# Optimization experiments

Measured on AMD Instinct MI355X. Metric: run time of the kernel, lower is better.

## Reference

```python
import jax, jax.numpy as jnp
import numpy as np

NEG_INF = -1e9  # matches torch masked_fill value of -1000000000.0


def setup_inputs() -> dict:
    key = jax.random.key(0)
    k1, k2, k3, k4 = jax.random.split(key, 4)
    B, H, S, D = 4, 16, 2048, 128
    query = jax.random.normal(k1, (B, H, S, D), dtype=jnp.float32)
    key_t = jax.random.normal(k2, (B, H, S, D), dtype=jnp.float32)
    value = jax.random.normal(k3, (B, H, S, D), dtype=jnp.float32)
    mask = jax.random.randint(k4, (B, 1, 1, S), 0, 2, dtype=jnp.int32)
    return {"query": query, "key": key_t, "value": value, "mask": mask, "dropout": 0}


def reference(query, key, value, mask, dropout):
    # scores = Q K^T / sqrt(d_k)   [B,H,S,S]
    d_k = query.shape[-1]
    scores = jnp.einsum("bhqd,bhkd->bhqk", query, key) / jnp.sqrt(jnp.asarray(d_k, query.dtype))
    # masked_fill_(mask == 0, -1e9); mask broadcasts [B,1,1,S] -> [B,H,S,S]
    scores = jnp.where(mask == 0, jnp.asarray(NEG_INF, scores.dtype), scores)
    # dropout == 0 -> identity (deterministic reference / eval mode)
    attn = jax.nn.softmax(scores, axis=-1)
    return jnp.einsum("bhqk,bhkd->bhqd", attn, value)
```

## Files before the change

kernel.cpp:

```cpp
#include <hip/hip_runtime.h>
#include <hip/hip_bf16.h>

#define S_LEN 2048
#define D_DIM 128
#define QBLK 128
#define KVBLK 32
#define NT (S_LEN / KVBLK)
#define KCHUNK 8192
#define VCHUNK 8192
#define PRE_BYTES ((size_t)64 * NT * (KCHUNK + VCHUNK))

typedef __attribute__((ext_vector_type(8))) short short8v;
typedef __attribute__((ext_vector_type(16))) float f32x16;

static __device__ __forceinline__ unsigned f2bf2(float lo, float hi) {
    float2 f2; f2.x = lo; f2.y = hi;
    __hip_bfloat162 h2 = __float22bfloat162_rn(f2);
    unsigned r;
    __builtin_memcpy(&r, &h2, 4);
    return r;
}

static __device__ __forceinline__ void plswap(unsigned& a, unsigned& b) {
    auto r = __builtin_amdgcn_permlane32_swap(a, b, false, false);
    a = r[0]; b = r[1];
}
static __device__ __forceinline__ float plswap_sum(float x) {
    unsigned a = __float_as_uint(x), b = a;
    plswap(a, b);
    return __uint_as_float(a) + __uint_as_float(b);
}

static __device__ __forceinline__ void gload16(const void* g, void* l) {
    __builtin_amdgcn_global_load_lds(
        (const __attribute__((address_space(1))) unsigned int*)g,
        (__attribute__((address_space(3))) unsigned int*)l,
        16, 0, 0);
}

static __device__ __forceinline__ void stage8k(const unsigned char* g, unsigned char* l,
                                               int wv, int lane) {
#pragma unroll
    for (int i = 0; i < 2; ++i) {
        const int off = (wv * 2 + i) * 1024;
        gload16(g + off + lane * 16, l + off);
    }
}

#define VTS 133

__global__ __launch_bounds__(256) void preconv(
    const float* __restrict__ Kp, const float* __restrict__ Vp,
    unsigned short* __restrict__ Ko, unsigned short* __restrict__ Vo)
{
    __shared__ float vt[64 * VTS];
    const int tid = threadIdx.x;
    const int blk = blockIdx.x;
    const size_t gbase = (size_t)(blk >> 5) * S_LEN * D_DIM + (size_t)(blk & 31) * 64 * D_DIM;

#pragma unroll
    for (int i = 0; i < 8; ++i) {
        int idx = (tid + 256 * i) * 4;
        int row = idx >> 7, col = idx & 127;
        float4 v4 = *(const float4*)(Vp + gbase + idx);
        float* d = &vt[row * VTS + col];
        d[0] = v4.x; d[1] = v4.y; d[2] = v4.z; d[3] = v4.w;
    }

    unsigned short* kout = Ko + (size_t)blk * 8192;
#pragma unroll
    for (int i = 0; i < 4; ++i) {
        int o = tid + 256 * i;
        int row = o >> 4, bs = o & 15;
        int b = (bs & 8) | ((bs ^ row) & 7);
        const float* gp = Kp + gbase + row * D_DIM + 8 * b;
        float4 x = *(const float4*)gp;
        float4 y = *(const float4*)(gp + 4);
        uint4 w;
        w.x = f2bf2(x.x, x.y); w.y = f2bf2(x.z, x.w);
        w.z = f2bf2(y.x, y.y); w.w = f2bf2(y.z, y.w);
        *(uint4*)(kout + o * 8) = w;
    }
    __syncthreads();

    unsigned short* vout = Vo + (size_t)blk * 8192;
#pragma unroll
    for (int i = 0; i < 4; ++i) {
        int u = tid + 256 * i;
        int ch = u >> 9, r = u & 511;
        int d = r >> 2, bs = r & 3;
        int b = bs ^ ((d >> 1) & 3);
        const float* c0 = &vt[(ch * 32 + 8 * b) * VTS + d];
        uint4 w;
        w.x = f2bf2(c0[0 * VTS], c0[1 * VTS]);
        w.y = f2bf2(c0[2 * VTS], c0[3 * VTS]);
        w.z = f2bf2(c0[4 * VTS], c0[5 * VTS]);
        w.w = f2bf2(c0[6 * VTS], c0[7 * VTS]);
        *(uint4*)(vout + u * 8) = w;
    }
}

#define ASMEM (3 * KCHUNK + 3 * VCHUNK + 8192)

__global__ __launch_bounds__(256, 2) void sdpa_fwd_pre(
    const float* __restrict__ Qp, const unsigned short* __restrict__ Kpre,
    const unsigned short* __restrict__ Vpre, const int* __restrict__ Mp,
    float* __restrict__ Op)
{
    extern __shared__ unsigned char smem[];
    unsigned char* KbB = smem;
    unsigned char* VbB = smem + 3 * KCHUNK;
    float* blds = (float*)(smem + 3 * KCHUNK + 3 * VCHUNK);

    const int tid  = threadIdx.x;
    const int lane = tid & 63;
    const int wv   = tid >> 6;
    const int h    = lane >> 5;
    const int c31  = lane & 31;
    const int hrx  = h ^ (c31 & 7);
    const int vsx  = (c31 >> 1) & 3;
    const int lbid = ((blockIdx.x & 7) << 7) | (blockIdx.x >> 3);
    const int bh   = lbid >> 4;
    const int q0   = (lbid & 15) * QBLK;
    const int bb   = bh >> 4;
    const size_t base = (size_t)bh * S_LEN * D_DIM;
    const unsigned char* Kg = (const unsigned char*)Kpre + (size_t)bh * (NT * KCHUNK);
    const unsigned char* Vg = (const unsigned char*)Vpre + (size_t)bh * (NT * VCHUNK);

    constexpr float SC   = 0.08838834764831845f * 1.4426950408889634f;
    constexpr float NEGB = -1.4426950408889634e9f;
    constexpr float M2   = 16.0f;

    {
        const int* mp = Mp + bb * S_LEN;
#pragma unroll
        for (int i = 0; i < S_LEN / 256; ++i)
            blds[tid + 256 * i] = mp[tid + 256 * i] ? -M2 : NEGB;
    }

    short8v qf[8];
    {
        const float* qrp = Qp + base + (size_t)(q0 + 32 * wv + c31) * D_DIM;
#pragma unroll
        for (int kk = 0; kk < 8; ++kk) {
            float4 x = *(const float4*)(qrp + 16 * kk + 8 * h);
            float4 y = *(const float4*)(qrp + 16 * kk + 8 * h + 4);
            uint4 w;
            w.x = f2bf2(x.x * SC, x.y * SC); w.y = f2bf2(x.z * SC, x.w * SC);
            w.z = f2bf2(y.x * SC, y.y * SC); w.w = f2bf2(y.z * SC, y.w * SC);
            *(uint4*)&qf[kk] = w;
        }
    }

    stage8k(Kg, KbB, wv, lane);
    stage8k(Vg, VbB, wv, lane);
    stage8k(Kg + KCHUNK, KbB + KCHUNK, wv, lane);
    stage8k(Vg + VCHUNK, VbB + VCHUNK, wv, lane);
    asm volatile("s_waitcnt vmcnt(4) lgkmcnt(0)" ::: "memory");
    __builtin_amdgcn_s_barrier();

    f32x16 acc[4];
#pragma unroll
    for (int dt = 0; dt < 4; ++dt)
#pragma unroll
        for (int i = 0; i < 16; ++i) acc[dt][i] = 0.f;

    float lpart = 0.f;
    int cur = 0;

#pragma unroll 1
    for (int t0 = 0; t0 < NT; ++t0) {
        const unsigned char* KcB = KbB + cur * KCHUNK;
        const unsigned char* VcB = VbB + cur * VCHUNK;

        const bool pf = (t0 + 2 < NT);
        if (pf) {
            int stg = cur + 2; if (stg >= 3) stg -= 3;
            stage8k(Kg + (size_t)(t0 + 2) * KCHUNK, KbB + stg * KCHUNK, wv, lane);
            stage8k(Vg + (size_t)(t0 + 2) * VCHUNK, VbB + stg * VCHUNK, wv, lane);
        }

        f32x16 s;
        {
            const float* bp = blds + t0 * KVBLK + 4 * h;
#pragma unroll
            for (int t4 = 0; t4 < 4; ++t4) {
                float4 b4 = *(const float4*)(bp + 8 * t4);
                s[4 * t4 + 0] = b4.x; s[4 * t4 + 1] = b4.y;
                s[4 * t4 + 2] = b4.z; s[4 * t4 + 3] = b4.w;
            }
        }

        {
            const unsigned char* rowp = KcB + (c31 << 8);
#pragma unroll
            for (int kk = 0; kk < 8; ++kk) {
                const int bs = ((2 * kk) & 8) | (((2 * kk) & 7) ^ hrx);
                short8v kf = *(const short8v*)(rowp + (bs << 4));
                s = __builtin_amdgcn_mfma_f32_32x32x16_bf16(kf, qf[kk], s, 0, 0, 0);
            }
        }

        unsigned w0[4], w1[4];
#pragma unroll
        for (int t4 = 0; t4 < 4; ++t4) {
            float e0 = __builtin_amdgcn_exp2f(s[4 * t4 + 0]);
            float e1 = __builtin_amdgcn_exp2f(s[4 * t4 + 1]);
            float e2 = __builtin_amdgcn_exp2f(s[4 * t4 + 2]);
            float e3 = __builtin_amdgcn_exp2f(s[4 * t4 + 3]);
            w0[t4] = f2bf2(e0, e1);
            w1[t4] = f2bf2(e2, e3);
            lpart += (e0 + e1) + (e2 + e3);
        }

#pragma unroll
        for (int kk = 0; kk < 2; ++kk) {
            unsigned ax = w0[2 * kk], bx = w0[2 * kk + 1];
            plswap(ax, bx);
            unsigned ay = w1[2 * kk], by = w1[2 * kk + 1];
            plswap(ay, by);
            uint4 pw;
            pw.x = ax; pw.y = ay; pw.z = bx; pw.w = by;
            short8v pfv = *(short8v*)&pw;
            const int bs = (2 * kk + h) ^ vsx;
#pragma unroll
            for (int dt = 0; dt < 4; ++dt) {
                short8v vf = *(const short8v*)(VcB + ((32 * dt + c31) << 6) + (bs << 4));
                acc[dt] = __builtin_amdgcn_mfma_f32_32x32x16_bf16(vf, pfv, acc[dt], 0, 0, 0);
            }
        }

        if (pf) {
            asm volatile("s_waitcnt vmcnt(4)" ::: "memory");
        } else {
            asm volatile("s_waitcnt vmcnt(0)" ::: "memory");
        }
        __builtin_amdgcn_s_barrier();
        cur = (cur + 1 == 3) ? 0 : cur + 1;
    }

    const float linv = 1.0f / plswap_sum(lpart);
    float* sw = (float*)(smem + wv * (32 * 68 * 4));
#pragma unroll
    for (int ph = 0; ph < 2; ++ph) {
#pragma unroll
        for (int dp = 0; dp < 2; ++dp) {
            const int dtg = 2 * ph + dp;
#pragma unroll
            for (int r = 0; r < 16; ++r) {
                int dloc = 32 * dp + (r & 3) + 8 * (r >> 2) + 4 * h;
                sw[c31 * 68 + dloc] = acc[dtg][r] * linv;
            }
        }
#pragma unroll
        for (int it = 0; it < 8; ++it) {
            int f4 = lane + 64 * it;
            int qq = f4 >> 4, c4 = f4 & 15;
            float4 val = *(const float4*)&sw[qq * 68 + 4 * c4];
            *(float4*)(Op + base + (size_t)(q0 + 32 * wv + qq) * D_DIM + 64 * ph + 4 * c4) = val;
        }
    }
}

#define FBKV 64
#define FBNT (S_LEN / FBKV)
#define FBQB 128
#define KSTRIDE 136
#define VSTRIDE 72
#define KELEMS (FBKV * KSTRIDE)
#define VELEMS (D_DIM * VSTRIDE)
#define KBYTES (2 * KELEMS * 2)
#define VBYTES (2 * VELEMS * 2)
#define FBSMEM (KBYTES + VBYTES + S_LEN * 4)

struct KReg { float4 a[4][2]; };
struct VReg { float4 a[2][4]; };

static __device__ __forceinline__ void load_K(KReg& kr, const float* Kbase,
                                              int kv0, int kr0, int kc8) {
#pragma unroll
    for (int i = 0; i < 4; ++i) {
        const float* gp = Kbase + (size_t)(kv0 + kr0 + 16 * i) * D_DIM + 8 * kc8;
        kr.a[i][0] = *(const float4*)gp;
        kr.a[i][1] = *(const float4*)(gp + 4);
    }
}
static __device__ __forceinline__ void write_K(const KReg& kr, unsigned short* Kn,
                                               int kr0, int kc8) {
#pragma unroll
    for (int i = 0; i < 4; ++i) {
        uint4 w;
        w.x = f2bf2(kr.a[i][0].x, kr.a[i][0].y);
        w.y = f2bf2(kr.a[i][0].z, kr.a[i][0].w);
        w.z = f2bf2(kr.a[i][1].x, kr.a[i][1].y);
        w.w = f2bf2(kr.a[i][1].z, kr.a[i][1].w);
        *(uint4*)&Kn[(kr0 + 16 * i) * KSTRIDE + 8 * kc8] = w;
    }
}
static __device__ __forceinline__ void load_V(VReg& vr, const float* Vbase,
                                              int kv0, int vkq, int vdg) {
#pragma unroll
    for (int ii = 0; ii < 2; ++ii)
#pragma unroll
        for (int r = 0; r < 4; ++r)
            vr.a[ii][r] = *(const float4*)(Vbase + (size_t)(kv0 + 4 * vkq + 32 * ii + r) * D_DIM + 4 * vdg);
}
static __device__ __forceinline__ void write_V(const VReg& vr, unsigned short* Vn,
                                               int vkq, int vdg) {
#pragma unroll
    for (int ii = 0; ii < 2; ++ii) {
        const int kvb = 4 * vkq + 32 * ii;
        const int d0  = 4 * vdg;
        uint2 u;
        u.x = f2bf2(vr.a[ii][0].x, vr.a[ii][1].x); u.y = f2bf2(vr.a[ii][2].x, vr.a[ii][3].x);
        *(uint2*)&Vn[(d0 + 0) * VSTRIDE + kvb] = u;
        u.x = f2bf2(vr.a[ii][0].y, vr.a[ii][1].y); u.y = f2bf2(vr.a[ii][2].y, vr.a[ii][3].y);
        *(uint2*)&Vn[(d0 + 1) * VSTRIDE + kvb] = u;
        u.x = f2bf2(vr.a[ii][0].z, vr.a[ii][1].z); u.y = f2bf2(vr.a[ii][2].z, vr.a[ii][3].z);
        *(uint2*)&Vn[(d0 + 2) * VSTRIDE + kvb] = u;
        u.x = f2bf2(vr.a[ii][0].w, vr.a[ii][1].w); u.y = f2bf2(vr.a[ii][2].w, vr.a[ii][3].w);
        *(uint2*)&Vn[(d0 + 3) * VSTRIDE + kvb] = u;
    }
}

__global__ __launch_bounds__(256, 2) void sdpa_fwd_fb(
    const float* __restrict__ Qp, const float* __restrict__ Kp,
    const float* __restrict__ Vp, const int* __restrict__ Mp,
    float* __restrict__ Op)
{
    extern __shared__ unsigned char smem[];
    unsigned short* Kb   = (unsigned short*)smem;
    unsigned short* Vb   = (unsigned short*)(smem + KBYTES);
    float*          mlds = (float*)(smem + KBYTES + VBYTES);

    const int tid  = threadIdx.x;
    const int lane = tid & 63;
    const int wv   = tid >> 6;
    const int h    = lane >> 5;
    const int c31  = lane & 31;
    const int bid  = blockIdx.x;
    const int bh   = bid >> 4;
    const int q0   = (bid & 15) * FBQB;
    const int bb   = bh >> 4;
    const size_t base = (size_t)bh * S_LEN * D_DIM;

    constexpr float SC   = 0.08838834764831845f * 1.4426950408889634f;
    constexpr float NEGB = -1.4426950408889634e9f;
    constexpr float THR  = 11.541560327111708f;

    {
        const int* mp = Mp + bb * S_LEN;
#pragma unroll
        for (int i = 0; i < S_LEN / 256; ++i)
            mlds[tid + 256 * i] = mp[tid + 256 * i] ? 0.f : NEGB;
    }

    short8v qf[8];
    {
        const float* qrp = Qp + base + (size_t)(q0 + 32 * wv + c31) * D_DIM;
#pragma unroll
        for (int kk = 0; kk < 8; ++kk) {
            float4 x = *(const float4*)(qrp + 16 * kk + 8 * h);
            float4 y = *(const float4*)(qrp + 16 * kk + 8 * h + 4);
            uint4 w;
            w.x = f2bf2(x.x, x.y); w.y = f2bf2(x.z, x.w);
            w.z = f2bf2(y.x, y.y); w.w = f2bf2(y.z, y.w);
            *(uint4*)&qf[kk] = w;
        }
    }

    const int kc8 = tid & 15;
    const int kr0 = tid >> 4;
    const int vdg = tid & 31;
    const int vkq = tid >> 5;

    {
        KReg kr; VReg vr;
        load_K(kr, Kp + base, 0, kr0, kc8);
        load_V(vr, Vp + base, 0, vkq, vdg);
        write_K(kr, Kb, kr0, kc8);
        write_V(vr, Vb, vkq, vdg);
    }
    __syncthreads();

    f32x16 acc[4];
#pragma unroll
    for (int dt = 0; dt < 4; ++dt)
#pragma unroll
        for (int i = 0; i < 16; ++i) acc[dt][i] = 0.f;

    float m2 = -INFINITY;
    float lsum = 0.f;
    int cur = 0;

#pragma unroll 1
    for (int t0 = 0; t0 < FBNT; ++t0) {
        const int kv0 = t0 * FBKV;
        unsigned short* Kc = Kb + cur * KELEMS;
        unsigned short* Vc = Vb + cur * VELEMS;
        unsigned short* Kn = Kb + (cur ^ 1) * KELEMS;
        unsigned short* Vn = Vb + (cur ^ 1) * VELEMS;
        const bool pf = (t0 + 1 < FBNT);

        KReg kr; VReg vr;
        if (pf) {
            load_K(kr, Kp + base, kv0 + FBKV, kr0, kc8);
            load_V(vr, Vp + base, kv0 + FBKV, vkq, vdg);
        }

        f32x16 stc[2];
#pragma unroll
        for (int c = 0; c < 2; ++c) {
            f32x16 s;
#pragma unroll
            for (int i = 0; i < 16; ++i) s[i] = 0.f;
#pragma unroll
            for (int kk = 0; kk < 8; ++kk) {
                short8v kf = *(const short8v*)&Kc[(32 * c + c31) * KSTRIDE + 16 * kk + 8 * h];
                s = __builtin_amdgcn_mfma_f32_32x32x16_bf16(kf, qf[kk], s, 0, 0, 0);
            }
            stc[c] = s;
        }

        float p[2][16];
#pragma unroll
        for (int c = 0; c < 2; ++c)
#pragma unroll
            for (int t = 0; t < 4; ++t) {
                float4 b4 = *(const float4*)&mlds[kv0 + 32 * c + 8 * t + 4 * h];
                p[c][4 * t + 0] = fmaf(stc[c][4 * t + 0], SC, b4.x);
                p[c][4 * t + 1] = fmaf(stc[c][4 * t + 1], SC, b4.y);
                p[c][4 * t + 2] = fmaf(stc[c][4 * t + 2], SC, b4.z);
                p[c][4 * t + 3] = fmaf(stc[c][4 * t + 3], SC, b4.w);
            }

        float pmax = -INFINITY;
#pragma unroll
        for (int c = 0; c < 2; ++c)
#pragma unroll
            for (int r = 0; r < 16; ++r) pmax = fmaxf(pmax, p[c][r]);
        pmax = fmaxf(pmax, __shfl_xor(pmax, 32));
        if (!__all(pmax <= m2 + THR)) {
            float mnew = fmaxf(m2, pmax);
            float fr = __builtin_amdgcn_exp2f(m2 - mnew);
            m2 = mnew;
            lsum *= fr;
#pragma unroll
            for (int dt = 0; dt < 4; ++dt)
#pragma unroll
                for (int i = 0; i < 16; ++i) acc[dt][i] *= fr;
        }
        float ssum = 0.f;
#pragma unroll
        for (int c = 0; c < 2; ++c)
#pragma unroll
            for (int r = 0; r < 16; ++r) {
                float e = __builtin_amdgcn_exp2f(p[c][r] - m2);
                p[c][r] = e; ssum += e;
            }
        ssum += __shfl_xor(ssum, 32);
        lsum += ssum;

        unsigned w0[2][4], w1[2][4];
#pragma unroll
        for (int c = 0; c < 2; ++c)
#pragma unroll
            for (int t = 0; t < 4; ++t) {
                w0[c][t] = f2bf2(p[c][4 * t + 0], p[c][4 * t + 1]);
                w1[c][t] = f2bf2(p[c][4 * t + 2], p[c][4 * t + 3]);
            }

#pragma unroll
        for (int kk = 0; kk < 4; ++kk) {
            const int t0i = (2 * kk) & 3,     c0i = (2 * kk) >> 2;
            const int t1i = (2 * kk + 1) & 3, c1i = (2 * kk + 1) >> 2;
            unsigned own0 = h ? w0[c1i][t1i] : w0[c0i][t0i];
            unsigned own1 = h ? w1[c1i][t1i] : w1[c0i][t0i];
            unsigned snd0 = h ? w0[c0i][t0i] : w0[c1i][t1i];
            unsigned snd1 = h ? w1[c0i][t0i] : w1[c1i][t1i];
            unsigned r0 = __shfl_xor(snd0, 32);
            unsigned r1 = __shfl_xor(snd1, 32);
            uint4 pw;
            pw.x = h ? r0 : own0;  pw.y = h ? r1 : own1;
            pw.z = h ? own0 : r0;  pw.w = h ? own1 : r1;
            short8v pfv = *(short8v*)&pw;
#pragma unroll
            for (int dt = 0; dt < 4; ++dt) {
                short8v vf = *(const short8v*)&Vc[(32 * dt + c31) * VSTRIDE + 16 * kk + 8 * h];
                acc[dt] = __builtin_amdgcn_mfma_f32_32x32x16_bf16(vf, pfv, acc[dt], 0, 0, 0);
            }
        }

        if (pf) {
            write_K(kr, Kn, kr0, kc8);
            write_V(vr, Vn, vkq, vdg);
        }
        __syncthreads();
        cur ^= 1;
    }

    __syncthreads();
    const float linv = 1.0f / lsum;
    float* sw = (float*)(smem + wv * (32 * 68 * 4));
#pragma unroll
    for (int ph = 0; ph < 2; ++ph) {
#pragma unroll
        for (int dp = 0; dp < 2; ++dp) {
            const int dtg = 2 * ph + dp;
#pragma unroll
            for (int r = 0; r < 16; ++r) {
                int dloc = 32 * dp + (r & 3) + 8 * (r >> 2) + 4 * h;
                sw[c31 * 68 + dloc] = acc[dtg][r] * linv;
            }
        }
#pragma unroll
        for (int it = 0; it < 8; ++it) {
            int f4 = lane + 64 * it;
            int qq = f4 >> 4, c4 = f4 & 15;
            float4 val = *(const float4*)&sw[qq * 68 + 4 * c4];
            *(float4*)(Op + base + (size_t)(q0 + 32 * wv + qq) * D_DIM + 64 * ph + 4 * c4) = val;
        }
    }
}

extern "C" void kernel_launch(void* const* d_in, const int* in_sizes, int n_in,
                              void* d_out, int out_size, void* d_ws, size_t ws_size,
                              hipStream_t stream) {
    (void)in_sizes; (void)n_in; (void)out_size;
    const float* Q = (const float*)d_in[0];
    const float* K = (const float*)d_in[1];
    const float* V = (const float*)d_in[2];
    const int*   M = (const int*)d_in[3];
    float*       O = (float*)d_out;

    if (ws_size >= PRE_BYTES) {
        unsigned short* Kpre = (unsigned short*)d_ws;
        unsigned short* Vpre = (unsigned short*)((char*)d_ws + PRE_BYTES / 2);
        hipLaunchKernelGGL(preconv, dim3(64 * 32), dim3(256), 0, stream, K, V, Kpre, Vpre);
        hipLaunchKernelGGL(sdpa_fwd_pre, dim3(1024), dim3(256), ASMEM, stream,
                           Q, Kpre, Vpre, M, O);
    } else {
        hipLaunchKernelGGL(sdpa_fwd_fb, dim3(1024), dim3(256), FBSMEM, stream, Q, K, V, M, O);
    }
}
```

Measured before the change: 193.2 us.

## Pre-pack K/V in MFMA fragment order and load fragments directly from global

The preconversion kernel now writes K and V in per-lane MFMA fragment order, staging K through shared memory as well. The attention kernel drops the triple-buffered LDS staging with async global-to-LDS loads and barriers. Each wave loads its K and V fragments straight from global memory (L2) with coalesced 16-byte loads. This removes LDS traffic and per-tile block barriers, but loses explicit prefetch, so global latency is exposed unless occupancy hides it, and each of the four waves now reads K/V separately.

```diff
diff --git a/kernel.cpp b/kernel.cpp
--- a/kernel.cpp
+++ b/kernel.cpp
@@ -31,22 +31,6 @@
     return __uint_as_float(a) + __uint_as_float(b);
 }
 
-static __device__ __forceinline__ void gload16(const void* g, void* l) {
-    __builtin_amdgcn_global_load_lds(
-        (const __attribute__((address_space(1))) unsigned int*)g,
-        (__attribute__((address_space(3))) unsigned int*)l,
-        16, 0, 0);
-}
-
-static __device__ __forceinline__ void stage8k(const unsigned char* g, unsigned char* l,
-                                               int wv, int lane) {
-#pragma unroll
-    for (int i = 0; i < 2; ++i) {
-        const int off = (wv * 2 + i) * 1024;
-        gload16(g + off + lane * 16, l + off);
-    }
-}
-
 #define VTS 133
 
 __global__ __launch_bounds__(256) void preconv(
@@ -66,41 +50,56 @@
         float* d = &vt[row * VTS + col];
         d[0] = v4.x; d[1] = v4.y; d[2] = v4.z; d[3] = v4.w;
     }
+    __syncthreads();
+
+    unsigned short* vout = Vo + (size_t)blk * 8192;
+#pragma unroll
+    for (int i = 0; i < 4; ++i) {
+        int u = tid + 256 * i;
+        int ch = u >> 9, r = u & 511;
+        int st = r >> 6, ln = r & 63;
+        int kk = st >> 2, dt = st & 3;
+        int c31l = ln & 31, hh = ln >> 5;
+        int rb = ch * 32 + 16 * kk + 8 * hh;
+        int d  = 32 * dt + c31l;
+        const float* p0 = &vt[rb * VTS + d];
+        uint4 w;
+        w.x = f2bf2(p0[0 * VTS], p0[1 * VTS]);
+        w.y = f2bf2(p0[2 * VTS], p0[3 * VTS]);
+        w.z = f2bf2(p0[4 * VTS], p0[5 * VTS]);
+        w.w = f2bf2(p0[6 * VTS], p0[7 * VTS]);
+        *(uint4*)(vout + u * 8) = w;
+    }
+    __syncthreads();
+
+#pragma unroll
+    for (int i = 0; i < 8; ++i) {
+        int idx = (tid + 256 * i) * 4;
+        int row = idx >> 7, col = idx & 127;
+        float4 v4 = *(const float4*)(Kp + gbase + idx);
+        float* d = &vt[row * VTS + col];
+        d[0] = v4.x; d[1] = v4.y; d[2] = v4.z; d[3] = v4.w;
+    }
+    __syncthreads();
 
     unsigned short* kout = Ko + (size_t)blk * 8192;
 #pragma unroll
     for (int i = 0; i < 4; ++i) {
-        int o = tid + 256 * i;
-        int row = o >> 4, bs = o & 15;
-        int b = (bs & 8) | ((bs ^ row) & 7);
-        const float* gp = Kp + gbase + row * D_DIM + 8 * b;
-        float4 x = *(const float4*)gp;
-        float4 y = *(const float4*)(gp + 4);
+        int u = tid + 256 * i;
+        int ch = u >> 9, r = u & 511;
+        int kk = r >> 6, ln = r & 63;
+        int c31l = ln & 31, hh = ln >> 5;
+        const float* p0 = &vt[(ch * 32 + c31l) * VTS + 16 * kk + 8 * hh];
+        float4 x = *(const float4*)p0;
+        float4 y = *(const float4*)(p0 + 4);
         uint4 w;
         w.x = f2bf2(x.x, x.y); w.y = f2bf2(x.z, x.w);
         w.z = f2bf2(y.x, y.y); w.w = f2bf2(y.z, y.w);
-        *(uint4*)(kout + o * 8) = w;
-    }
-    __syncthreads();
-
-    unsigned short* vout = Vo + (size_t)blk * 8192;
-#pragma unroll
-    for (int i = 0; i < 4; ++i) {
-        int u = tid + 256 * i;
-        int ch = u >> 9, r = u & 511;
-        int d = r >> 2, bs = r & 3;
-        int b = bs ^ ((d >> 1) & 3);
-        const float* c0 = &vt[(ch * 32 + 8 * b) * VTS + d];
-        uint4 w;
-        w.x = f2bf2(c0[0 * VTS], c0[1 * VTS]);
-        w.y = f2bf2(c0[2 * VTS], c0[3 * VTS]);
-        w.z = f2bf2(c0[4 * VTS], c0[5 * VTS]);
-        w.w = f2bf2(c0[6 * VTS], c0[7 * VTS]);
-        *(uint4*)(vout + u * 8) = w;
-    }
-}
-
-#define ASMEM (3 * KCHUNK + 3 * VCHUNK + 8192)
+        *(uint4*)(kout + u * 8) = w;
+    }
+}
+
+#define ASMEM (8192 + 4 * 8704)
 
 __global__ __launch_bounds__(256, 2) void sdpa_fwd_pre(
     const float* __restrict__ Qp, const unsigned short* __restrict__ Kpre,
@@ -108,17 +107,13 @@
     float* __restrict__ Op)
 {
     extern __shared__ unsigned char smem[];
-    unsigned char* KbB = smem;
-    unsigned char* VbB = smem + 3 * KCHUNK;
-    float* blds = (float*)(smem + 3 * KCHUNK + 3 * VCHUNK);
+    float* blds = (float*)smem;
 
     const int tid  = threadIdx.x;
     const int lane = tid & 63;
     const int wv   = tid >> 6;
     const int h    = lane >> 5;
     const int c31  = lane & 31;
-    const int hrx  = h ^ (c31 & 7);
-    const int vsx  = (c31 >> 1) & 3;
     const int lbid = ((blockIdx.x & 7) << 7) | (blockIdx.x >> 3);
     const int bh   = lbid >> 4;
     const int q0   = (lbid & 15) * QBLK;
@@ -151,13 +146,7 @@
             *(uint4*)&qf[kk] = w;
         }
     }
-
-    stage8k(Kg, KbB, wv, lane);
-    stage8k(Vg, VbB, wv, lane);
-    stage8k(Kg + KCHUNK, KbB + KCHUNK, wv, lane);
-    stage8k(Vg + VCHUNK, VbB + VCHUNK, wv, lane);
-    asm volatile("s_waitcnt vmcnt(4) lgkmcnt(0)" ::: "memory");
-    __builtin_amdgcn_s_barrier();
+    __syncthreads();
 
     f32x16 acc[4];
 #pragma unroll
@@ -166,19 +155,16 @@
         for (int i = 0; i < 16; ++i) acc[dt][i] = 0.f;
 
     float lpart = 0.f;
-    int cur = 0;
 
 #pragma unroll 1
     for (int t0 = 0; t0 < NT; ++t0) {
-        const unsigned char* KcB = KbB + cur * KCHUNK;
-        const unsigned char* VcB = VbB + cur * VCHUNK;
-
-        const bool pf = (t0 + 2 < NT);
-        if (pf) {
-            int stg = cur + 2; if (stg >= 3) stg -= 3;
-            stage8k(Kg + (size_t)(t0 + 2) * KCHUNK, KbB + stg * KCHUNK, wv, lane);
-            stage8k(Vg + (size_t)(t0 + 2) * VCHUNK, VbB + stg * VCHUNK, wv, lane);
-        }
+        const unsigned char* kimg = Kg + (size_t)t0 * KCHUNK;
+        const unsigned char* vimg = Vg + (size_t)t0 * VCHUNK;
+
+        short8v kf[8];
+#pragma unroll
+        for (int kk = 0; kk < 8; ++kk)
+            kf[kk] = *(const short8v*)(kimg + ((kk * 64 + lane) << 4));
 
         f32x16 s;
         {
@@ -191,15 +177,14 @@
             }
         }
 
-        {
-            const unsigned char* rowp = KcB + (c31 << 8);
-#pragma unroll
-            for (int kk = 0; kk < 8; ++kk) {
-                const int bs = ((2 * kk) & 8) | (((2 * kk) & 7) ^ hrx);
-                short8v kf = *(const short8v*)(rowp + (bs << 4));
-                s = __builtin_amdgcn_mfma_f32_32x32x16_bf16(kf, qf[kk], s, 0, 0, 0);
-            }
-        }
+#pragma unroll
+        for (int kk = 0; kk < 8; ++kk)
+            s = __builtin_amdgcn_mfma_f32_32x32x16_bf16(kf[kk], qf[kk], s, 0, 0, 0);
+
+        short8v vf[8];
+#pragma unroll
+        for (int st = 0; st < 8; ++st)
+            vf[st] = *(const short8v*)(vimg + ((st * 64 + lane) << 4));
 
         unsigned w0[4], w1[4];
 #pragma unroll
@@ -222,25 +207,14 @@
             uint4 pw;
             pw.x = ax; pw.y = ay; pw.z = bx; pw.w = by;
             short8v pfv = *(short8v*)&pw;
-            const int bs = (2 * kk + h) ^ vsx;
-#pragma unroll
-            for (int dt = 0; dt < 4; ++dt) {
-                short8v vf = *(const short8v*)(VcB + ((32 * dt + c31) << 6) + (bs << 4));
-                acc[dt] = __builtin_amdgcn_mfma_f32_32x32x16_bf16(vf, pfv, acc[dt], 0, 0, 0);
-            }
-        }
-
-        if (pf) {
-            asm volatile("s_waitcnt vmcnt(4)" ::: "memory");
-        } else {
-            asm volatile("s_waitcnt vmcnt(0)" ::: "memory");
-        }
-        __builtin_amdgcn_s_barrier();
-        cur = (cur + 1 == 3) ? 0 : cur + 1;
+#pragma unroll
+            for (int dt = 0; dt < 4; ++dt)
+                acc[dt] = __builtin_amdgcn_mfma_f32_32x32x16_bf16(vf[4 * kk + dt], pfv, acc[dt], 0, 0, 0);
+        }
     }
 
     const float linv = 1.0f / plswap_sum(lpart);
-    float* sw = (float*)(smem + wv * (32 * 68 * 4));
+    float* sw = (float*)(smem + 8192 + wv * 8704);
 #pragma unroll
     for (int ph = 0; ph < 2; ++ph) {
 #pragma unroll
```

Measured after the change: 229.8 us. +19.0%, slower.
